# Kernel optimization log

Measured on AMD Instinct MI355X. Metric: run time of the kernel, lower is better.

Reference implementation:

```python
import jax, jax.numpy as jnp
import numpy as np

H = 1024
E = 8
TOP_K = 2


def setup_inputs() -> dict:
    key = jax.random.key(0)
    ks = jax.random.split(key, 6)
    B, S = 4, 2048
    hidden_states = jax.random.normal(ks[0], (B, S, H), dtype=jnp.float32)
    # router weight, init N(0, 0.02)
    router_w = jax.random.normal(ks[1], (E, H), dtype=jnp.float32) * 0.02
    # stacked expert FFN params (nn.Linear: y = x @ W.T + b)
    lim = 1.0 / np.sqrt(H)
    W1 = jax.random.uniform(ks[2], (E, H, H), minval=-lim, maxval=lim, dtype=jnp.float32)
    b1 = jax.random.uniform(ks[3], (E, H), minval=-lim, maxval=lim, dtype=jnp.float32)
    W2 = jax.random.uniform(ks[4], (E, H, H), minval=-lim, maxval=lim, dtype=jnp.float32)
    b2 = jax.random.uniform(ks[5], (E, H), minval=-lim, maxval=lim, dtype=jnp.float32)
    return {"hidden_states": hidden_states, "router_w": router_w,
            "W1": W1, "b1": b1, "W2": W2, "b2": b2}


def reference(hidden_states, router_w, W1, b1, W2, b2):
    B, S, _ = hidden_states.shape
    # ---- router ----
    logits = jnp.einsum('bsh,eh->bse', hidden_states, router_w)  # [B,S,E]
    router_probs = jax.nn.softmax(logits.astype(jnp.float32), axis=-1)
    top_vals, top_idx = jax.lax.top_k(router_probs, TOP_K)        # [B,S,K]
    top_vals = top_vals / jnp.sum(top_vals, axis=-1, keepdims=True)  # norm_topk_prob
    # per-token per-expert combine weight (sum of top-k weights matching expert)
    w = jnp.sum(jax.nn.one_hot(top_idx, E, dtype=top_vals.dtype) * top_vals[..., None], axis=-2)  # [B,S,E]
    # ---- dense all-expert FFN (faithful to reference: every expert on every token) ----
    h1 = jax.nn.relu(jnp.einsum('bsh,efh->bsef', hidden_states, W1) + b1)   # [B,S,E,F]
    expert_out = jnp.einsum('bsef,egf->bseg', h1, W2) + b2                  # [B,S,E,H]
    moe_out = jnp.einsum('bseh,bse->bsh', expert_out, w)
    return hidden_states + moe_out, router_probs
```

## Files before the change

kernel.cpp:

```cpp
#include <hip/hip_runtime.h>
#include <hip/hip_bf16.h>


#define HD   1024
#define NTOK 8192
#define NEXP 8
#define BM   128
#define BN   128
#define BK   64
#define ZROW 8192
#define MAXP 17408
#define EP_LDSW 136

typedef __attribute__((ext_vector_type(8))) short  vshort8;
typedef __attribute__((ext_vector_type(4))) short  vshort4;
typedef __attribute__((ext_vector_type(4))) float  vfloat4;

typedef __attribute__((address_space(1))) const unsigned gas_uint;
typedef __attribute__((address_space(3))) unsigned       las_uint;

__device__ __forceinline__ void gld16(const void* g, void* l) {
    __builtin_amdgcn_global_load_lds((gas_uint*)g, (las_uint*)l, 16, 0, 0);
}

__device__ __forceinline__ short bf16r(float f) {
    union { float f; unsigned u; } a; a.f = f;
    unsigned r = a.u + 0x7FFFu + ((a.u >> 16) & 1u);
    return (short)(r >> 16);
}

__global__ void init_kernel(int* counts, int* fill, int* pair_token, short* xb) {
    int i = blockIdx.x * 256 + threadIdx.x;
    if (i < NEXP) { counts[i] = 0; fill[i] = 0; }
    if (i < MAXP) pair_token[i] = ZROW;
    if (i < HD / 8) {
        vshort8 z = {0, 0, 0, 0, 0, 0, 0, 0};
        *(vshort8*)(xb + (size_t)ZROW * HD + i * 8) = z;
    }
}

__global__ __launch_bounds__(256) void router_kernel(
    const float* __restrict__ x, const float* __restrict__ rw,
    float* __restrict__ out, short* __restrict__ xb,
    float* __restrict__ probs_out, int2* __restrict__ tok_top,
    float2* __restrict__ tok_w, int* __restrict__ counts) {
    __shared__ float rws[NEXP * HD];
    __shared__ int hist[NEXP];
    int t = threadIdx.x;
    if (t < NEXP) hist[t] = 0;
    for (int j = 0; j < 8; ++j) {
        int idx = j * 1024 + t * 4;
        *(vfloat4*)(rws + idx) = *(const vfloat4*)(rw + idx);
    }
    __syncthreads();
    int wave = t >> 6, lane = t & 63;
    for (int it = 0; it < 8; ++it) {
        int token = blockIdx.x * 32 + it * 4 + wave;
        const float* xr = x + (size_t)token * HD;
        float part[NEXP];
#pragma unroll
        for (int e = 0; e < NEXP; ++e) part[e] = 0.f;
        for (int j = 0; j < 4; ++j) {
            int off = j * 256 + lane * 4;
            vfloat4 xv = *(const vfloat4*)(xr + off);
            *(vfloat4*)(out + (size_t)token * HD + off) = xv;
            vshort4 bq;
            bq.x = bf16r(xv.x); bq.y = bf16r(xv.y); bq.z = bf16r(xv.z); bq.w = bf16r(xv.w);
            *(vshort4*)(xb + (size_t)token * HD + off) = bq;
#pragma unroll
            for (int e = 0; e < NEXP; ++e) {
                vfloat4 wv = *(const vfloat4*)(rws + e * HD + off);
                part[e] += xv.x * wv.x + xv.y * wv.y + xv.z * wv.z + xv.w * wv.w;
            }
        }
#pragma unroll
        for (int e = 0; e < NEXP; ++e)
            for (int off = 32; off; off >>= 1)
                part[e] += __shfl_xor(part[e], off, 64);
        if (lane == 0) {
            float m = part[0];
#pragma unroll
            for (int e = 1; e < NEXP; ++e) m = fmaxf(m, part[e]);
            float p[NEXP], s = 0.f;
#pragma unroll
            for (int e = 0; e < NEXP; ++e) { p[e] = expf(part[e] - m); s += p[e]; }
            float inv = 1.f / s;
#pragma unroll
            for (int e = 0; e < NEXP; ++e) {
                p[e] *= inv;
                probs_out[(size_t)token * NEXP + e] = p[e];
            }
            int i0 = 0;
#pragma unroll
            for (int e = 1; e < NEXP; ++e) if (p[e] > p[i0]) i0 = e;
            int i1 = (i0 == 0) ? 1 : 0;
#pragma unroll
            for (int e = 0; e < NEXP; ++e) if (e != i0 && p[e] > p[i1]) i1 = e;
            float s2 = 1.f / (p[i0] + p[i1]);
            tok_top[token] = make_int2(i0, i1);
            tok_w[token]   = make_float2(p[i0] * s2, p[i1] * s2);
            atomicAdd(&hist[i0], 1);
            atomicAdd(&hist[i1], 1);
        }
    }
    __syncthreads();
    if (t < NEXP) atomicAdd(&counts[t], hist[t]);
}

__global__ __launch_bounds__(256) void scatter_kernel(
    const int2* __restrict__ tok_top, const float2* __restrict__ tok_w,
    const int* __restrict__ counts, int* fill,
    int* __restrict__ pair_token, float* __restrict__ pair_w) {
    __shared__ int lhist[NEXP];
    __shared__ int lbase[NEXP];
    int t = threadIdx.x;
    if (t < NEXP) lhist[t] = 0;
    __syncthreads();
    int offs[NEXP];
    {
        int acc = 0;
#pragma unroll
        for (int f = 0; f < NEXP; ++f) {
            offs[f] = acc;
            acc += (counts[f] + 127) & ~127;
        }
    }
    int token = blockIdx.x * 256 + t;
    int2 ti = tok_top[token];
    float2 tw = tok_w[token];
    int r0 = atomicAdd(&lhist[ti.x], 1);
    int r1 = atomicAdd(&lhist[ti.y], 1);
    __syncthreads();
    if (t < NEXP) lbase[t] = atomicAdd(&fill[t], lhist[t]);
    __syncthreads();
    int s0 = offs[ti.x] + lbase[ti.x] + r0;
    pair_token[s0] = token; pair_w[s0] = tw.x;
    int s1 = offs[ti.y] + lbase[ti.y] + r1;
    pair_token[s1] = token; pair_w[s1] = tw.y;
}

__global__ void convw_kernel(const float* __restrict__ W1, const float* __restrict__ W2,
                             short* __restrict__ D1, short* __restrict__ D2) {
    size_t t = (size_t)blockIdx.x * 256 + threadIdx.x;
    const size_t PER = (size_t)NEXP * HD * HD / 8;
    const float* src = W1; short* dst = D1;
    if (t >= PER) { t -= PER; src = W2; dst = D2; }
    size_t C = t >> 6;
    int l  = (int)(t & 63);
    int kc = (int)(C & 31);
    int ng = (int)((C >> 5) & 63);
    int ei = (int)(C >> 11);
    int n = ng * 16 + (l & 15);
    int k = kc * 32 + (l >> 4) * 8;
    const float* s = src + ((size_t)ei * HD + n) * HD + k;
    vfloat4 a = *(const vfloat4*)s;
    vfloat4 b = *(const vfloat4*)(s + 4);
    vshort8 o;
    o[0] = bf16r(a.x); o[1] = bf16r(a.y); o[2] = bf16r(a.z); o[3] = bf16r(a.w);
    o[4] = bf16r(b.x); o[5] = bf16r(b.y); o[6] = bf16r(b.z); o[7] = bf16r(b.w);
    *(vshort8*)(dst + t * 8) = o;
}

template <int MODE>
__global__ __launch_bounds__(512, 4) void moe_gemm(
    const short* __restrict__ A, const short* __restrict__ Bw,
    const float* __restrict__ bias, const int* __restrict__ pair_token,
    const float* __restrict__ pair_w, const int* __restrict__ counts,
    short* __restrict__ h1sw_out, float* __restrict__ out) {
    __shared__ short smem[(MODE == 0) ? (BM * EP_LDSW) : (2 * BM * BK)];

    const int row0 = blockIdx.x * BM;
    int e = 0;
    {
        int csum = 0;
#pragma unroll
        for (int f = 0; f < NEXP; ++f) {
            int p = (counts[f] + 127) & ~127;
            if (csum + p <= row0) e = f + 1;
            csum += p;
        }
        if (row0 >= csum) return;
    }

    const int t = threadIdx.x;
    const int wave = t >> 6, lane = t & 63;
    const int wm = wave >> 2, wn = wave & 3;
    const int quad = lane >> 4, l16 = lane & 15;
    const int colb = blockIdx.y * BN;

    const char* agp;
    if (MODE == 0) {
        int tok = pair_token[row0 + wave * 16 + l16];
        agp = (const char*)A + (size_t)tok * (HD * 2) + quad * 16;
    } else {
        agp = (const char*)A + (((size_t)(row0 >> 4) + wave) * 32) * 1024 + lane * 16;
    }
    const char* bgp = (const char*)Bw +
        (((size_t)e * 64 + (colb >> 4) + wave) * 32) * 1024 + lane * 16;

    vfloat4 acc[4][2];
#pragma unroll
    for (int i = 0; i < 4; ++i)
#pragma unroll
        for (int j = 0; j < 2; ++j)
            acc[i][j] = (vfloat4){0.f, 0.f, 0.f, 0.f};

    for (int k0 = 0; k0 < HD; k0 += BK) {
        __syncthreads();
        const int kc = k0 >> 5;
#pragma unroll
        for (int s = 0; s < 2; ++s) {
            const char* ga = (MODE == 0)
                ? (agp + (size_t)k0 * 2 + s * 64)
                : (agp + (size_t)(kc + s) * 1024);
            gld16(ga, smem + (wave * 2 + s) * 512);
            gld16(bgp + (size_t)(kc + s) * 1024, smem + 8192 + (wave * 2 + s) * 512);
        }
        __syncthreads();
#pragma unroll
        for (int s = 0; s < 2; ++s) {
            vshort8 af[4], bfr[2];
#pragma unroll
            for (int i = 0; i < 4; ++i)
                af[i] = *(const vshort8*)(smem + ((wm * 4 + i) * 2 + s) * 512 + lane * 8);
#pragma unroll
            for (int j = 0; j < 2; ++j)
                bfr[j] = *(const vshort8*)(smem + 8192 + ((wn * 2 + j) * 2 + s) * 512 + lane * 8);
#pragma unroll
            for (int i = 0; i < 4; ++i)
#pragma unroll
                for (int j = 0; j < 2; ++j)
                    acc[i][j] = __builtin_amdgcn_mfma_f32_16x16x32_bf16(af[i], bfr[j], acc[i][j], 0, 0, 0);
        }
    }

    if (MODE == 0) {
        __syncthreads();
#pragma unroll
        for (int j = 0; j < 2; ++j) {
            int col = wn * 32 + j * 16 + l16;
            float bv = bias[e * HD + colb + col];
#pragma unroll
            for (int i = 0; i < 4; ++i) {
                int rl = wm * 64 + i * 16 + quad * 4;
#pragma unroll
                for (int reg = 0; reg < 4; ++reg) {
                    float v = acc[i][j][reg] + bv;
                    v = v > 0.f ? v : 0.f;
                    smem[(rl + reg) * EP_LDSW + col] = bf16r(v);
                }
            }
        }
        __syncthreads();
        int lrow = wave * 16 + l16;
#pragma unroll
        for (int kk = 0; kk < 4; ++kk) {
            vshort8 v = *(const vshort8*)(smem + lrow * EP_LDSW + kk * 32 + quad * 8);
            size_t chunk = ((size_t)((row0 >> 4) + wave) * 32) + ((colb >> 5) + kk);
            *(vshort8*)(h1sw_out + chunk * 512 + lane * 8) = v;
        }
    } else {
        int tok[4][4]; float wv[4][4];
#pragma unroll
        for (int i = 0; i < 4; ++i)
#pragma unroll
            for (int reg = 0; reg < 4; ++reg) {
                int r = row0 + wm * 64 + i * 16 + quad * 4 + reg;
                tok[i][reg] = pair_token[r];
                wv[i][reg] = pair_w[r];
            }
#pragma unroll
        for (int j = 0; j < 2; ++j) {
            int col = colb + wn * 32 + j * 16 + l16;
            float bv = bias[e * HD + col];
#pragma unroll
            for (int i = 0; i < 4; ++i)
#pragma unroll
                for (int reg = 0; reg < 4; ++reg)
                    if (tok[i][reg] < ZROW)
                        atomicAdd(out + (size_t)tok[i][reg] * HD + col,
                                  wv[i][reg] * (acc[i][j][reg] + bv));
        }
    }
}

extern "C" void kernel_launch(void* const* d_in, const int* in_sizes, int n_in,
                              void* d_out, int out_size, void* d_ws, size_t ws_size,
                              hipStream_t stream) {
    const float* x  = (const float*)d_in[0];
    const float* rw = (const float*)d_in[1];
    const float* W1 = (const float*)d_in[2];
    const float* b1 = (const float*)d_in[3];
    const float* W2 = (const float*)d_in[4];
    const float* b2 = (const float*)d_in[5];
    float* out   = (float*)d_out;
    float* probs = out + (size_t)NTOK * HD;

    char* ws = (char*)d_ws;
    short* xb = (short*)ws;            ws += (size_t)(NTOK + 1) * HD * 2;
    short* h1 = (short*)ws;            ws += (size_t)MAXP * HD * 2;
    int*   pair_token = (int*)ws;      ws += MAXP * 4;
    float* pair_w     = (float*)ws;    ws += MAXP * 4;
    int*   counts = (int*)ws;          ws += 256;
    int*   fill   = (int*)ws;          ws += 256;
    int2*   tok_top = (int2*)ws;       ws += NTOK * 8;
    float2* tok_w   = (float2*)ws;     ws += NTOK * 8;
    short* w1sw = (short*)ws;          ws += (size_t)NEXP * HD * HD * 2;
    short* w2sw = (short*)ws;          ws += (size_t)NEXP * HD * HD * 2;
    (void)ws_size;

    init_kernel<<<MAXP / 256, 256, 0, stream>>>(counts, fill, pair_token, xb);
    router_kernel<<<NTOK / 32, 256, 0, stream>>>(x, rw, out, xb, probs,
                                                 tok_top, tok_w, counts);
    scatter_kernel<<<NTOK / 256, 256, 0, stream>>>(tok_top, tok_w, counts, fill,
                                                   pair_token, pair_w);
    int cg = (int)(2 * ((size_t)NEXP * HD * HD / 8) / 256);
    convw_kernel<<<cg, 256, 0, stream>>>(W1, W2, w1sw, w2sw);
    dim3 gg(MAXP / BM, HD / BN);
    moe_gemm<0><<<gg, 512, 0, stream>>>(xb, w1sw, b1, pair_token, pair_w, counts, h1, nullptr);
    moe_gemm<1><<<gg, 512, 0, stream>>>(h1, w2sw, b2, pair_token, pair_w, counts, nullptr, out);
}
```

Measured before the change: 326.2 us.

## Drop LDS staging in MoE GEMM, use register prefetch, merge weight conversion

The MoE GEMM no longer stages A/B tiles in LDS through global_load_lds. Each of 4 waves now loads its MFMA fragments straight from global memory into registers, with a one-step register prefetch and a 4x4 accumulator tile per wave. The block shrinks from 512 to 256 threads. The weight conversion kernel is folded into the router kernel as extra blocks that write the same swizzled layout with a reordered read pattern, saving a launch. There is no tile sharing between waves, so global traffic per block rises and more load is put on L2, while block barriers are removed.

```diff
diff --git a/kernel.cpp b/kernel.cpp
--- a/kernel.cpp
+++ b/kernel.cpp
@@ -7,21 +7,14 @@
 #define NEXP 8
 #define BM   128
 #define BN   128
-#define BK   64
 #define ZROW 8192
 #define MAXP 17408
 #define EP_LDSW 136
+#define RB   256
 
 typedef __attribute__((ext_vector_type(8))) short  vshort8;
 typedef __attribute__((ext_vector_type(4))) short  vshort4;
 typedef __attribute__((ext_vector_type(4))) float  vfloat4;
-
-typedef __attribute__((address_space(1))) const unsigned gas_uint;
-typedef __attribute__((address_space(3))) unsigned       las_uint;
-
-__device__ __forceinline__ void gld16(const void* g, void* l) {
-    __builtin_amdgcn_global_load_lds((gas_uint*)g, (las_uint*)l, 16, 0, 0);
-}
 
 __device__ __forceinline__ short bf16r(float f) {
     union { float f; unsigned u; } a; a.f = f;
@@ -39,14 +32,35 @@
     }
 }
 
-__global__ __launch_bounds__(256) void router_kernel(
+__global__ __launch_bounds__(256) void prep_kernel(
     const float* __restrict__ x, const float* __restrict__ rw,
+    const float* __restrict__ W1, const float* __restrict__ W2,
     float* __restrict__ out, short* __restrict__ xb,
     float* __restrict__ probs_out, int2* __restrict__ tok_top,
-    float2* __restrict__ tok_w, int* __restrict__ counts) {
+    float2* __restrict__ tok_w, int* __restrict__ counts,
+    short* __restrict__ w1sw, short* __restrict__ w2sw) {
     __shared__ float rws[NEXP * HD];
     __shared__ int hist[NEXP];
     int t = threadIdx.x;
+    if (blockIdx.x >= RB) {
+        size_t u = (size_t)(blockIdx.x - RB) * 256 + t;
+        const size_t PER = (size_t)NEXP * HD * HD / 8;
+        const float* src = W1; short* dst = w1sw;
+        if (u >= PER) { u -= PER; src = W2; dst = w2sw; }
+        size_t s = u * 8;
+        int e  = (int)(s >> 20);
+        int n  = (int)((s >> 10) & 1023);
+        int k  = (int)(s & 1023);
+        vfloat4 a = *(const vfloat4*)(src + s);
+        vfloat4 b = *(const vfloat4*)(src + s + 4);
+        vshort8 o;
+        o[0] = bf16r(a.x); o[1] = bf16r(a.y); o[2] = bf16r(a.z); o[3] = bf16r(a.w);
+        o[4] = bf16r(b.x); o[5] = bf16r(b.y); o[6] = bf16r(b.z); o[7] = bf16r(b.w);
+        size_t chunk = ((size_t)e * 64 + (n >> 4)) * 32 + (k >> 5);
+        int lane = ((k >> 3) & 3) * 16 + (n & 15);
+        *(vshort8*)(dst + chunk * 512 + lane * 8) = o;
+        return;
+    }
     if (t < NEXP) hist[t] = 0;
     for (int j = 0; j < 8; ++j) {
         int idx = j * 1024 + t * 4;
@@ -139,35 +153,13 @@
     pair_token[s1] = token; pair_w[s1] = tw.y;
 }
 
-__global__ void convw_kernel(const float* __restrict__ W1, const float* __restrict__ W2,
-                             short* __restrict__ D1, short* __restrict__ D2) {
-    size_t t = (size_t)blockIdx.x * 256 + threadIdx.x;
-    const size_t PER = (size_t)NEXP * HD * HD / 8;
-    const float* src = W1; short* dst = D1;
-    if (t >= PER) { t -= PER; src = W2; dst = D2; }
-    size_t C = t >> 6;
-    int l  = (int)(t & 63);
-    int kc = (int)(C & 31);
-    int ng = (int)((C >> 5) & 63);
-    int ei = (int)(C >> 11);
-    int n = ng * 16 + (l & 15);
-    int k = kc * 32 + (l >> 4) * 8;
-    const float* s = src + ((size_t)ei * HD + n) * HD + k;
-    vfloat4 a = *(const vfloat4*)s;
-    vfloat4 b = *(const vfloat4*)(s + 4);
-    vshort8 o;
-    o[0] = bf16r(a.x); o[1] = bf16r(a.y); o[2] = bf16r(a.z); o[3] = bf16r(a.w);
-    o[4] = bf16r(b.x); o[5] = bf16r(b.y); o[6] = bf16r(b.z); o[7] = bf16r(b.w);
-    *(vshort8*)(dst + t * 8) = o;
-}
-
 template <int MODE>
-__global__ __launch_bounds__(512, 4) void moe_gemm(
+__global__ __launch_bounds__(256, 2) void moe_gemm(
     const short* __restrict__ A, const short* __restrict__ Bw,
     const float* __restrict__ bias, const int* __restrict__ pair_token,
     const float* __restrict__ pair_w, const int* __restrict__ counts,
     short* __restrict__ h1sw_out, float* __restrict__ out) {
-    __shared__ short smem[(MODE == 0) ? (BM * EP_LDSW) : (2 * BM * BK)];
+    __shared__ short smem[(MODE == 0) ? (BM * EP_LDSW) : 16];
 
     const int row0 = blockIdx.x * BM;
     int e = 0;
@@ -184,61 +176,60 @@
 
     const int t = threadIdx.x;
     const int wave = t >> 6, lane = t & 63;
-    const int wm = wave >> 2, wn = wave & 3;
+    const int wm = wave >> 1, wn = wave & 1;
     const int quad = lane >> 4, l16 = lane & 15;
     const int colb = blockIdx.y * BN;
 
-    const char* agp;
+    const short* aRow[4];
+#pragma unroll
+    for (int i = 0; i < 4; ++i) {
+        if (MODE == 0) {
+            int tok = pair_token[row0 + wm * 64 + i * 16 + l16];
+            aRow[i] = A + (size_t)tok * HD + quad * 8;
+        } else {
+            aRow[i] = A + ((size_t)(row0 >> 4) + wm * 4 + i) * 16384 + lane * 8;
+        }
+    }
+    const short* bRow[4];
+#pragma unroll
+    for (int j = 0; j < 4; ++j)
+        bRow[j] = Bw + ((size_t)e * 64 + (colb >> 4) + wn * 4 + j) * 16384 + lane * 8;
+
+    vfloat4 acc[4][4];
+#pragma unroll
+    for (int i = 0; i < 4; ++i)
+#pragma unroll
+        for (int j = 0; j < 4; ++j)
+            acc[i][j] = (vfloat4){0.f, 0.f, 0.f, 0.f};
+
+    vshort8 aP[4], bP[4], aN[4], bN[4];
+#pragma unroll
+    for (int i = 0; i < 4; ++i) {
+        aP[i] = *(const vshort8*)(aRow[i]);
+        bP[i] = *(const vshort8*)(bRow[i]);
+    }
+#pragma unroll 4
+    for (int kc = 0; kc < 32; ++kc) {
+        if (kc < 31) {
+#pragma unroll
+            for (int i = 0; i < 4; ++i) {
+                aN[i] = *(const vshort8*)(aRow[i] + (MODE == 0 ? (kc + 1) * 32 : (kc + 1) * 512));
+                bN[i] = *(const vshort8*)(bRow[i] + (kc + 1) * 512);
+            }
+        }
+#pragma unroll
+        for (int i = 0; i < 4; ++i)
+#pragma unroll
+            for (int j = 0; j < 4; ++j)
+                acc[i][j] = __builtin_amdgcn_mfma_f32_16x16x32_bf16(aP[i], bP[j], acc[i][j], 0, 0, 0);
+#pragma unroll
+        for (int i = 0; i < 4; ++i) { aP[i] = aN[i]; bP[i] = bN[i]; }
+    }
+
     if (MODE == 0) {
-        int tok = pair_token[row0 + wave * 16 + l16];
-        agp = (const char*)A + (size_t)tok * (HD * 2) + quad * 16;
-    } else {
-        agp = (const char*)A + (((size_t)(row0 >> 4) + wave) * 32) * 1024 + lane * 16;
-    }
-    const char* bgp = (const char*)Bw +
-        (((size_t)e * 64 + (colb >> 4) + wave) * 32) * 1024 + lane * 16;
-
-    vfloat4 acc[4][2];
-#pragma unroll
-    for (int i = 0; i < 4; ++i)
-#pragma unroll
-        for (int j = 0; j < 2; ++j)
-            acc[i][j] = (vfloat4){0.f, 0.f, 0.f, 0.f};
-
-    for (int k0 = 0; k0 < HD; k0 += BK) {
-        __syncthreads();
-        const int kc = k0 >> 5;
-#pragma unroll
-        for (int s = 0; s < 2; ++s) {
-            const char* ga = (MODE == 0)
-                ? (agp + (size_t)k0 * 2 + s * 64)
-                : (agp + (size_t)(kc + s) * 1024);
-            gld16(ga, smem + (wave * 2 + s) * 512);
-            gld16(bgp + (size_t)(kc + s) * 1024, smem + 8192 + (wave * 2 + s) * 512);
-        }
-        __syncthreads();
-#pragma unroll
-        for (int s = 0; s < 2; ++s) {
-            vshort8 af[4], bfr[2];
-#pragma unroll
-            for (int i = 0; i < 4; ++i)
-                af[i] = *(const vshort8*)(smem + ((wm * 4 + i) * 2 + s) * 512 + lane * 8);
-#pragma unroll
-            for (int j = 0; j < 2; ++j)
-                bfr[j] = *(const vshort8*)(smem + 8192 + ((wn * 2 + j) * 2 + s) * 512 + lane * 8);
-#pragma unroll
-            for (int i = 0; i < 4; ++i)
-#pragma unroll
-                for (int j = 0; j < 2; ++j)
-                    acc[i][j] = __builtin_amdgcn_mfma_f32_16x16x32_bf16(af[i], bfr[j], acc[i][j], 0, 0, 0);
-        }
-    }
-
-    if (MODE == 0) {
-        __syncthreads();
-#pragma unroll
-        for (int j = 0; j < 2; ++j) {
-            int col = wn * 32 + j * 16 + l16;
+#pragma unroll
+        for (int j = 0; j < 4; ++j) {
+            int col = wn * 64 + j * 16 + l16;
             float bv = bias[e * HD + colb + col];
 #pragma unroll
             for (int i = 0; i < 4; ++i) {
@@ -252,12 +243,16 @@
             }
         }
         __syncthreads();
-        int lrow = wave * 16 + l16;
-#pragma unroll
-        for (int kk = 0; kk < 4; ++kk) {
-            vshort8 v = *(const vshort8*)(smem + lrow * EP_LDSW + kk * 32 + quad * 8);
-            size_t chunk = ((size_t)((row0 >> 4) + wave) * 32) + ((colb >> 5) + kk);
-            *(vshort8*)(h1sw_out + chunk * 512 + lane * 8) = v;
+#pragma unroll
+        for (int u = 0; u < 2; ++u) {
+            int sgl = wave * 2 + u;
+            int lrow = sgl * 16 + l16;
+#pragma unroll
+            for (int kk = 0; kk < 4; ++kk) {
+                vshort8 v = *(const vshort8*)(smem + lrow * EP_LDSW + kk * 32 + quad * 8);
+                size_t chunk = ((size_t)((row0 >> 4) + sgl) * 32) + ((colb >> 5) + kk);
+                *(vshort8*)(h1sw_out + chunk * 512 + lane * 8) = v;
+            }
         }
     } else {
         int tok[4][4]; float wv[4][4];
@@ -270,8 +265,8 @@
                 wv[i][reg] = pair_w[r];
             }
 #pragma unroll
-        for (int j = 0; j < 2; ++j) {
-            int col = colb + wn * 32 + j * 16 + l16;
+        for (int j = 0; j < 4; ++j) {
+            int col = colb + wn * 64 + j * 16 + l16;
             float bv = bias[e * HD + col];
 #pragma unroll
             for (int i = 0; i < 4; ++i)
@@ -310,13 +305,12 @@
     (void)ws_size;
 
     init_kernel<<<MAXP / 256, 256, 0, stream>>>(counts, fill, pair_token, xb);
-    router_kernel<<<NTOK / 32, 256, 0, stream>>>(x, rw, out, xb, probs,
-                                                 tok_top, tok_w, counts);
+    int swb = (int)(2 * ((size_t)NEXP * HD * HD / 8) / 256);
+    prep_kernel<<<RB + swb, 256, 0, stream>>>(x, rw, W1, W2, out, xb, probs,
+                                              tok_top, tok_w, counts, w1sw, w2sw);
     scatter_kernel<<<NTOK / 256, 256, 0, stream>>>(tok_top, tok_w, counts, fill,
                                                    pair_token, pair_w);
-    int cg = (int)(2 * ((size_t)NEXP * HD * HD / 8) / 256);
-    convw_kernel<<<cg, 256, 0, stream>>>(W1, W2, w1sw, w2sw);
     dim3 gg(MAXP / BM, HD / BN);
-    moe_gemm<0><<<gg, 512, 0, stream>>>(xb, w1sw, b1, pair_token, pair_w, counts, h1, nullptr);
-    moe_gemm<1><<<gg, 512, 0, stream>>>(h1, w2sw, b2, pair_token, pair_w, counts, nullptr, out);
-}
+    moe_gemm<0><<<gg, 256, 0, stream>>>(xb, w1sw, b1, pair_token, pair_w, counts, h1, nullptr);
+    moe_gemm<1><<<gg, 256, 0, stream>>>(h1, w2sw, b2, pair_token, pair_w, counts, nullptr, out);
+}
```

New measurement: 384.1 us. 1.18x slower.
